# Optimization experiments

Measured on AMD Instinct MI355X. Metric: run time of the kernel, lower is better.

The kernel has to match this reference:

```python
import jax, jax.numpy as jnp
import numpy as np

H = 100  # LSTM hidden size


def setup_inputs() -> dict:
    key = jax.random.key(0)
    ks = jax.random.split(key, 9)
    T, B, I = 2048, 128, 1
    s = 0.1
    return {
        "input_seq": jax.random.normal(ks[0], (T, B, I), dtype=jnp.float32),
        "W_ih": jax.random.normal(ks[1], (4 * H, I), dtype=jnp.float32) * s,
        "W_hh": jax.random.normal(ks[2], (4 * H, H), dtype=jnp.float32) * s,
        "b_ih": jax.random.normal(ks[3], (4 * H,), dtype=jnp.float32) * s,
        "b_hh": jax.random.normal(ks[4], (4 * H,), dtype=jnp.float32) * s,
        "W1": jax.random.normal(ks[5], (64, H), dtype=jnp.float32) * s,
        "b1": jax.random.normal(ks[6], (64,), dtype=jnp.float32) * s,
        "W2": jax.random.normal(ks[7], (1, 64), dtype=jnp.float32) * s,
        "b2": jax.random.normal(ks[8], (1,), dtype=jnp.float32) * s,
    }


def _lstm_scan(x, W_ih, W_hh, b_ih, b_hh):
    # x: [T, B, I]. PyTorch gate order: i, f, g, o.
    T, B, _ = x.shape
    b = b_ih + b_hh
    # precompute input contribution for all timesteps: [T, B, 4H]
    xg = jnp.einsum('tbi,gi->tbg', x, W_ih) + b

    def step(carry, xg_t):
        h, c = carry
        gates = xg_t + h @ W_hh.T  # [B, 4H]
        i = jax.nn.sigmoid(gates[:, 0 * H:1 * H])
        f = jax.nn.sigmoid(gates[:, 1 * H:2 * H])
        g = jnp.tanh(gates[:, 2 * H:3 * H])
        o = jax.nn.sigmoid(gates[:, 3 * H:4 * H])
        c = f * c + i * g
        h = o * jnp.tanh(c)
        return (h, c), h

    h0 = jnp.zeros((B, H), dtype=x.dtype)
    c0 = jnp.zeros((B, H), dtype=x.dtype)
    _, hs = jax.lax.scan(step, (h0, c0), xg)
    return hs  # [T, B, H]


def reference(input_seq, W_ih, W_hh, b_ih, b_hh, W1, b1, W2, b2):
    hs = _lstm_scan(input_seq, W_ih, W_hh, b_ih, b_hh)  # [T, B, H]
    lin = hs @ W1.T + b1          # [T, B, 64]
    out = lin @ W2.T + b2         # [T, B, 1]
    return out[-1, 0]             # [1] — matches lin_out[-1][0]
```

## Files before the change

### kernel.cpp

```cpp
#include <hip/hip_runtime.h>
#include <hip/hip_fp16.h>

#define T_STEPS 2048
#define BATCH   128
#define HID     100
#define KP      128
#define NTH     448

#define LOG2E 1.44269504088896340736f

typedef int   i32x8 __attribute__((ext_vector_type(8)));
typedef float f32x4 __attribute__((ext_vector_type(4)));

__global__ __launch_bounds__(NTH)
void lstm_caviar_kernel(
    const float* __restrict__ x,
    const float* __restrict__ W_ih,
    const float* __restrict__ W_hh,
    const float* __restrict__ b_ih,
    const float* __restrict__ b_hh,
    const float* __restrict__ W1,
    const float* __restrict__ b1,
    const float* __restrict__ W2,
    const float* __restrict__ b2,
    float* __restrict__ out)
{
    __shared__ __align__(32) unsigned char hbuf[2][KP];
    __shared__ float hfin[KP];
    __shared__ float x_lds[T_STEPS];
    __shared__ float red_lds[64];

    const int tid  = threadIdx.x;
    const int w    = tid >> 6;
    const int c16  = tid & 15;
    const int l16  = (tid >> 4) & 3;
    const int unit = w * 16 + c16;
    const bool uvalid = (unit < HID);
    const bool writer = (l16 == 0) && uvalid;

    for (int t = tid; t < T_STEPS; t += NTH)
        x_lds[t] = x[t * BATCH];
    if (tid < KP) { hbuf[0][tid] = 0; hbuf[1][tid] = 0; }

    i32x8 bfr[4];
    float nwig[4], nbsg[4];
    #pragma unroll
    for (int g = 0; g < 4; ++g) {
        const int r = g * HID + (uvalid ? unit : 0);
        const float Lg = (g == 2) ? (2.0f * LOG2E) : LOG2E;
        i32x8 f;
        #pragma unroll
        for (int d = 0; d < 8; ++d) {
            const int k0 = l16 * 32 + d * 4;
            float v0 = 0.f, v1 = 0.f, v2 = 0.f, v3 = 0.f;
            if (uvalid) {
                if (k0     < HID) v0 = Lg * W_hh[r * HID + k0];
                if (k0 + 1 < HID) v1 = Lg * W_hh[r * HID + k0 + 1];
                if (k0 + 2 < HID) v2 = Lg * W_hh[r * HID + k0 + 2];
                if (k0 + 3 < HID) v3 = Lg * W_hh[r * HID + k0 + 3];
            }
            int reg = __builtin_amdgcn_cvt_pk_fp8_f32(v0, v1, 0,   false);
            reg     = __builtin_amdgcn_cvt_pk_fp8_f32(v2, v3, reg, true);
            f[d] = reg;
        }
        bfr[g] = f;
        nwig[g] = uvalid ? -Lg * W_ih[r] : 0.0f;
        nbsg[g] = uvalid ? -Lg * (b_ih[r] + b_hh[r]) : 0.0f;
    }

    float c = 0.0f;
    float h = 0.0f;
    const int aoff = l16 * 32;
    const f32x4 czero = {0.f, 0.f, 0.f, 0.f};
    __syncthreads();

    auto step = [&](const unsigned char* hb, unsigned char* hn, const float xt) {
        const float np0 = fmaf(nwig[0], xt, nbsg[0]);
        const float np1 = fmaf(nwig[1], xt, nbsg[1]);
        const float np2 = fmaf(nwig[2], xt, nbsg[2]);
        const float np3 = fmaf(nwig[3], xt, nbsg[3]);

        const i32x8 av = *(const i32x8*)(hb + aoff);

        const f32x4 ai = __builtin_amdgcn_mfma_scale_f32_16x16x128_f8f6f4(
                 av, bfr[0], czero, 0, 0, 0, 0x7F7F7F7F, 0, 0x7F7F7F7F);
        const f32x4 af = __builtin_amdgcn_mfma_scale_f32_16x16x128_f8f6f4(
                 av, bfr[1], czero, 0, 0, 0, 0x7F7F7F7F, 0, 0x7F7F7F7F);
        const f32x4 ag = __builtin_amdgcn_mfma_scale_f32_16x16x128_f8f6f4(
                 av, bfr[2], czero, 0, 0, 0, 0x7F7F7F7F, 0, 0x7F7F7F7F);
        const f32x4 ao = __builtin_amdgcn_mfma_scale_f32_16x16x128_f8f6f4(
                 av, bfr[3], czero, 0, 0, 0, 0x7F7F7F7F, 0, 0x7F7F7F7F);

        const float ii = __builtin_amdgcn_rcpf(1.0f + __builtin_amdgcn_exp2f(np0 - ai[0]));
        const float ff = __builtin_amdgcn_rcpf(1.0f + __builtin_amdgcn_exp2f(np1 - af[0]));
        const float gt = fmaf(2.0f, __builtin_amdgcn_rcpf(1.0f + __builtin_amdgcn_exp2f(np2 - ag[0])), -1.0f);
        c = fmaf(ff, c, ii * gt);
        const float th = fmaf(2.0f, __builtin_amdgcn_rcpf(1.0f + __builtin_amdgcn_exp2f(-2.0f * LOG2E * c)), -1.0f);
        const float oo = __builtin_amdgcn_rcpf(1.0f + __builtin_amdgcn_exp2f(np3 - ao[0]));
        h = oo * th;

        if (writer) {
            const int pk = __builtin_amdgcn_cvt_pk_fp8_f32(h, 0.0f, 0, false);
            hn[unit] = (unsigned char)(pk & 0xFF);
        }
        __syncthreads();
    };

    for (int t = 0; t < T_STEPS; t += 2) {
        step(hbuf[0], hbuf[1], x_lds[t]);
        step(hbuf[1], hbuf[0], x_lds[t + 1]);
    }

    if (writer) hfin[unit] = h;
    if (tid >= HID && tid < KP) hfin[tid] = 0.0f;
    __syncthreads();

    if (tid < 64) {
        const float* rw = W1 + tid * HID;
        float a = 0.0f;
        for (int k = 0; k < HID; ++k)
            a = fmaf(rw[k], hfin[k], a);
        red_lds[tid] = a + b1[tid];
    }
    __syncthreads();
    if (tid == 0) {
        float a = b2[0];
        for (int k = 0; k < 64; ++k)
            a = fmaf(W2[k], red_lds[k], a);
        out[0] = a;
    }
}

extern "C" void kernel_launch(void* const* d_in, const int* in_sizes, int n_in,
                              void* d_out, int out_size, void* d_ws, size_t ws_size,
                              hipStream_t stream) {
    lstm_caviar_kernel<<<1, NTH, 0, stream>>>(
        (const float*)d_in[0],
        (const float*)d_in[1],
        (const float*)d_in[2],
        (const float*)d_in[3],
        (const float*)d_in[4],
        (const float*)d_in[5],
        (const float*)d_in[6],
        (const float*)d_in[7],
        (const float*)d_in[8],
        (float*)d_out);
}
```

Baseline: 740.8 us.

## Spread LSTM gates across lanes and recombine with DPP quad broadcasts

The weight-fragment layout is remapped so each lane of the MFMA output owns one gate of one hidden unit, and all 64 lanes in a wave now produce useful gate values instead of only one output row. Each lane computes a single sigmoid or tanh activation, and DPP quad-permute moves gather the i, f, g and o values within each 4-lane group for the cell update. This shortens the serial transcendental chain per step, at the cost of lane selects, DPP moves, and redundant c/h computation across the quad.

```diff
diff --git a/kernel.cpp b/kernel.cpp
--- a/kernel.cpp
+++ b/kernel.cpp
@@ -11,6 +11,12 @@
 
 typedef int   i32x8 __attribute__((ext_vector_type(8)));
 typedef float f32x4 __attribute__((ext_vector_type(4)));
+
+template <int CTRL>
+__device__ __forceinline__ float dpp_mov(float v) {
+    int y = __builtin_amdgcn_update_dpp(0, __float_as_int(v), CTRL, 0xF, 0xF, true);
+    return __int_as_float(y);
+}
 
 __global__ __launch_bounds__(NTH)
 void lstm_caviar_kernel(
@@ -32,28 +38,32 @@
 
     const int tid  = threadIdx.x;
     const int w    = tid >> 6;
-    const int c16  = tid & 15;
+    const int n    = tid & 15;
+    const int gate = n & 3;
+    const int usub = n >> 2;
     const int l16  = (tid >> 4) & 3;
-    const int unit = w * 16 + c16;
+    const int unit = w * 16 + l16 * 4 + usub;
     const bool uvalid = (unit < HID);
-    const bool writer = (l16 == 0) && uvalid;
+    const bool writer = (gate == 0) && uvalid;
+    const bool is_g   = (gate == 2);
 
     for (int t = tid; t < T_STEPS; t += NTH)
         x_lds[t] = x[t * BATCH];
     if (tid < KP) { hbuf[0][tid] = 0; hbuf[1][tid] = 0; }
 
     i32x8 bfr[4];
-    float nwig[4], nbsg[4];
     #pragma unroll
-    for (int g = 0; g < 4; ++g) {
-        const int r = g * HID + (uvalid ? unit : 0);
-        const float Lg = (g == 2) ? (2.0f * LOG2E) : LOG2E;
+    for (int q = 0; q < 4; ++q) {
+        const int uu = w * 16 + q * 4 + usub;
+        const bool uv = (uu < HID);
+        const int r  = gate * HID + (uv ? uu : 0);
+        const float Lg = is_g ? (2.0f * LOG2E) : LOG2E;
         i32x8 f;
         #pragma unroll
         for (int d = 0; d < 8; ++d) {
             const int k0 = l16 * 32 + d * 4;
             float v0 = 0.f, v1 = 0.f, v2 = 0.f, v3 = 0.f;
-            if (uvalid) {
+            if (uv) {
                 if (k0     < HID) v0 = Lg * W_hh[r * HID + k0];
                 if (k0 + 1 < HID) v1 = Lg * W_hh[r * HID + k0 + 1];
                 if (k0 + 2 < HID) v2 = Lg * W_hh[r * HID + k0 + 2];
@@ -63,41 +73,52 @@
             reg     = __builtin_amdgcn_cvt_pk_fp8_f32(v2, v3, reg, true);
             f[d] = reg;
         }
-        bfr[g] = f;
-        nwig[g] = uvalid ? -Lg * W_ih[r] : 0.0f;
-        nbsg[g] = uvalid ? -Lg * (b_ih[r] + b_hh[r]) : 0.0f;
+        bfr[q] = f;
     }
+    const int rown = gate * HID + (uvalid ? unit : 0);
+    const float Lgo = is_g ? (2.0f * LOG2E) : LOG2E;
+    const float nwi = uvalid ? -Lgo * W_ih[rown] : 0.0f;
+    const float nbs = uvalid ? -Lgo * (b_ih[rown] + b_hh[rown]) : 0.0f;
 
     float c = 0.0f;
     float h = 0.0f;
     const int aoff = l16 * 32;
     const f32x4 czero = {0.f, 0.f, 0.f, 0.f};
+    const bool lb0 = (l16 & 1) != 0;
+    const bool lb1 = (l16 & 2) != 0;
     __syncthreads();
 
     auto step = [&](const unsigned char* hb, unsigned char* hn, const float xt) {
-        const float np0 = fmaf(nwig[0], xt, nbsg[0]);
-        const float np1 = fmaf(nwig[1], xt, nbsg[1]);
-        const float np2 = fmaf(nwig[2], xt, nbsg[2]);
-        const float np3 = fmaf(nwig[3], xt, nbsg[3]);
+        const float np = fmaf(nwi, xt, nbs);
 
         const i32x8 av = *(const i32x8*)(hb + aoff);
 
-        const f32x4 ai = __builtin_amdgcn_mfma_scale_f32_16x16x128_f8f6f4(
+        const f32x4 a0 = __builtin_amdgcn_mfma_scale_f32_16x16x128_f8f6f4(
                  av, bfr[0], czero, 0, 0, 0, 0x7F7F7F7F, 0, 0x7F7F7F7F);
-        const f32x4 af = __builtin_amdgcn_mfma_scale_f32_16x16x128_f8f6f4(
+        const f32x4 a1 = __builtin_amdgcn_mfma_scale_f32_16x16x128_f8f6f4(
                  av, bfr[1], czero, 0, 0, 0, 0x7F7F7F7F, 0, 0x7F7F7F7F);
-        const f32x4 ag = __builtin_amdgcn_mfma_scale_f32_16x16x128_f8f6f4(
+        const f32x4 a2 = __builtin_amdgcn_mfma_scale_f32_16x16x128_f8f6f4(
                  av, bfr[2], czero, 0, 0, 0, 0x7F7F7F7F, 0, 0x7F7F7F7F);
-        const f32x4 ao = __builtin_amdgcn_mfma_scale_f32_16x16x128_f8f6f4(
+        const f32x4 a3 = __builtin_amdgcn_mfma_scale_f32_16x16x128_f8f6f4(
                  av, bfr[3], czero, 0, 0, 0, 0x7F7F7F7F, 0, 0x7F7F7F7F);
 
-        const float ii = __builtin_amdgcn_rcpf(1.0f + __builtin_amdgcn_exp2f(np0 - ai[0]));
-        const float ff = __builtin_amdgcn_rcpf(1.0f + __builtin_amdgcn_exp2f(np1 - af[0]));
-        const float gt = fmaf(2.0f, __builtin_amdgcn_rcpf(1.0f + __builtin_amdgcn_exp2f(np2 - ag[0])), -1.0f);
-        c = fmaf(ff, c, ii * gt);
-        const float th = fmaf(2.0f, __builtin_amdgcn_rcpf(1.0f + __builtin_amdgcn_exp2f(-2.0f * LOG2E * c)), -1.0f);
-        const float oo = __builtin_amdgcn_rcpf(1.0f + __builtin_amdgcn_exp2f(np3 - ao[0]));
-        h = oo * th;
+        const float t0  = lb0 ? a1[0] : a0[0];
+        const float t1  = lb0 ? a3[0] : a2[0];
+        const float raw = lb1 ? t1 : t0;
+
+        const float e   = __builtin_amdgcn_exp2f(np - raw);
+        const float r   = __builtin_amdgcn_rcpf(1.0f + e);
+        const float act = is_g ? fmaf(2.0f, r, -1.0f) : r;
+
+        const float ig = dpp_mov<0x00>(act);
+        const float fg = dpp_mov<0x55>(act);
+        const float gg = dpp_mov<0xAA>(act);
+        const float og = dpp_mov<0xFF>(act);
+
+        c = fmaf(fg, c, ig * gg);
+        const float th = fmaf(2.0f, __builtin_amdgcn_rcpf(
+                              1.0f + __builtin_amdgcn_exp2f(-2.0f * LOG2E * c)), -1.0f);
+        h = og * th;
 
         if (writer) {
             const int pk = __builtin_amdgcn_cvt_pk_fp8_f32(h, 0.0f, 0, false);
```

Measured after the change: 672.4 us. 1.1x faster.
